# Kernel tuning notes

Hardware: AMD Instinct MI355X
Metric: run time of the kernel (lower is better)

Reference implementation:

```python
import jax, jax.numpy as jnp
import numpy as np
from jax import lax

C_IN = 256
C_OUT = 256
KS = 3


def _conv(x, w, b):
    # x: [B,C,H,W], w: [O,I,kh,kw] -> NCHW 'SAME' conv, stride 1
    y = lax.conv_general_dilated(x, w, window_strides=(1, 1), padding='SAME',
                                 dimension_numbers=('NCHW', 'OIHW', 'NCHW'))
    return y + b[None, :, None, None]


def setup_inputs() -> dict:
    key = jax.random.key(0)
    ks = jax.random.split(key, 7)
    B, H, W = 2, 64, 64
    fan = C_IN * KS * KS
    lim = float(np.sqrt(6.0 / (fan + C_OUT * KS * KS)))  # xavier uniform
    return {
        'x': jax.random.normal(ks[0], (B, C_IN, H, W), jnp.float32),
        'ref_x': jax.random.normal(ks[1], (B, C_IN, H, W), jnp.float32),
        'conv1_w': jax.random.uniform(ks[2], (C_OUT, C_IN, KS, KS), jnp.float32, -lim, lim),
        'conv1_b': jnp.zeros((C_OUT,), jnp.float32),
        'conv2_w': jax.random.uniform(ks[3], (C_OUT, C_IN, KS, KS), jnp.float32, -lim, lim),
        'conv2_b': jnp.zeros((C_OUT,), jnp.float32),
        'gamma': jnp.array([0.5], jnp.float32),
    }


def reference(x, ref_x, conv1_w, conv1_b, conv2_w, conv2_b, gamma):
    B, Cin, H, W = x.shape
    HW = H * W
    x_f = jax.nn.relu(_conv(x, conv1_w, conv1_b)).reshape(B, C_OUT, HW)        # [B,C,HW]
    r_f = jax.nn.relu(_conv(ref_x, conv1_w, conv1_b))                          # [B,C,H,W]
    r_f = r_f.transpose(0, 2, 3, 1).reshape(B, HW, C_OUT)                      # [B,HW,C]
    corr = jnp.einsum('bnc,bcm->bnm', r_f, x_f)                                # [B,HW,HW]
    corr = jax.nn.softmax(corr, axis=1)                                        # softmax over ref positions
    ref_c2 = jax.nn.relu(_conv(x, conv2_w, conv2_b)).reshape(B, C_OUT, HW)     # [B,C,HW]
    A = jnp.einsum('bcn,bnm->bcm', ref_c2, corr).reshape(x.shape)              # [B,C,H,W]
    return A * gamma[0] + x
```

## Files before the change

kernel.cpp:

```cpp
#include <hip/hip_runtime.h>
#include <hip/hip_bf16.h>

#define B_ 2
#define C_ 256
#define H_ 64
#define W_ 64
#define N_ 4096

typedef short bf16x8 __attribute__((ext_vector_type(8)));
typedef _Float16 f16x8 __attribute__((ext_vector_type(8)));
typedef float f32x4 __attribute__((ext_vector_type(4)));
typedef float f32x16 __attribute__((ext_vector_type(16)));

static __device__ __forceinline__ unsigned short f2bf(float f) {
    union { float f; unsigned u; } uf; uf.f = f;
    unsigned r = uf.u + 0x7fffu + ((uf.u >> 16) & 1u);
    return (unsigned short)(r >> 16);
}
static __device__ __forceinline__ unsigned short f2h_u(float f) {
    union { _Float16 h; unsigned short u; } c; c.h = (_Float16)f; return c.u;
}

static __device__ __forceinline__ void gload16(const void* g, void* l) {
    __builtin_amdgcn_global_load_lds(
        (const __attribute__((address_space(1))) unsigned int*)g,
        (__attribute__((address_space(3))) unsigned int*)l, 16, 0, 0);
}

__global__ __launch_bounds__(256) void cvt_x_k(const float* __restrict__ x,
                                               const float* __restrict__ ref_x,
                                               unsigned short* __restrict__ xtx,
                                               unsigned short* __restrict__ xtr)
{
    __shared__ unsigned short t[64][72];
    const int pt = blockIdx.x, ct = blockIdx.y;
    const int which = blockIdx.z >> 1, b = blockIdx.z & 1;
    const float* in = which ? ref_x : x;
    unsigned short* out = which ? xtr : xtx;
    const int a = threadIdx.x & 63, r = threadIdx.x >> 6;
    #pragma unroll
    for (int i = 0; i < 16; ++i) {
        int c = i * 4 + r;
        t[c][a] = f2h_u(in[((size_t)(b * C_ + ct * 64 + c) << 12) + pt * 64 + a]);
    }
    __syncthreads();
    #pragma unroll
    for (int i = 0; i < 16; ++i) {
        int p = i * 4 + r;
        out[((size_t)(b * N_ + pt * 64 + p) << 8) + ct * 64 + a] = t[a][p];
    }
}

__global__ __launch_bounds__(256) void cvt_w_k(const float* __restrict__ w1,
                                               const float* __restrict__ w2,
                                               unsigned short* __restrict__ wh1,
                                               unsigned short* __restrict__ wh2)
{
    int g = blockIdx.x;
    const float* w = (g < 2304) ? w1 : w2;
    unsigned short* wh = (g < 2304) ? wh1 : wh2;
    int i = (g % 2304) * 256 + threadIdx.x;
    int ci = i & 255, co = (i >> 8) & 255, tap = i >> 16;
    wh[i] = f2h_u(w[((size_t)(co * 256 + ci)) * 9 + tap]);
}

__global__ __launch_bounds__(256) void conv_mfma_k(
    const unsigned short* __restrict__ xtx, const unsigned short* __restrict__ xtr,
    const unsigned short* __restrict__ w1h, const unsigned short* __restrict__ w2h,
    const float* __restrict__ b1, const float* __restrict__ b2,
    unsigned short* __restrict__ f1x, unsigned short* __restrict__ f1r,
    unsigned short* __restrict__ f2)
{
    __shared__ unsigned short As[4 * 576 * 8];
    __shared__ unsigned short Bs[4 * 66 * 32];
    const int tid = threadIdx.x;
    const int pt  = blockIdx.x;
    const int cot = blockIdx.y;
    const int cid = blockIdx.z >> 1;
    const int b   = blockIdx.z & 1;

    const unsigned short* xt = (cid == 1) ? xtr : xtx;
    const unsigned short* wt = (cid == 2) ? w2h : w1h;
    const float* bias = (cid == 2) ? b2 : b1;
    unsigned short* out = (cid == 0) ? f1x : (cid == 1) ? f1r : f2;
    const int trans = (cid != 2);

    const int lane = tid & 63, wid = tid >> 6;
    const int wco = wid >> 1, wpos = wid & 1;
    const int rl = lane & 15, q = lane >> 4;
    const int r0 = pt * 2;

    f32x4 acc[2][4];
    #pragma unroll
    for (int mi = 0; mi < 2; ++mi)
        #pragma unroll
        for (int ni = 0; ni < 4; ++ni)
            #pragma unroll
            for (int e = 0; e < 4; ++e) acc[mi][ni][e] = 0.f;

    for (int k0 = 0; k0 < C_; k0 += 32) {
        #pragma unroll
        for (int tap = 0; tap < 9; ++tap) {
            gload16(wt + ((size_t)(tap * C_ + cot * 64 + lane) << 8) + k0 + wid * 8,
                    &As[(wid * 576 + tap * 64 + lane) * 8]);
        }
        #pragma unroll
        for (int j = 0; j < 5; ++j) {
            int it = tid + j * 256;
            if (it < 1056) {
                int col = it >> 4, sub = it & 15;
                int row = sub >> 2, qb = sub & 3;
                int h = r0 + row - 1, c = col - 1;
                float4 v; v.x = 0.f; v.y = 0.f; v.z = 0.f; v.w = 0.f;
                if (h >= 0 && h < 64 && c >= 0 && c < 64)
                    v = *(const float4*)(xt + ((size_t)(b * N_ + h * 64 + c) << 8) + k0 + qb * 8);
                int chunk = qb ^ ((col >> 1) & 3);
                *(float4*)&Bs[(row * 66 + col) * 32 + chunk * 8] = v;
            }
        }
        __syncthreads();

        #pragma unroll
        for (int tap = 0; tap < 9; ++tap) {
            const int kh = tap / 3, kw = tap % 3;
            f16x8 a0 = *(const f16x8*)&As[(q * 576 + tap * 64 + wco * 32 + rl) * 8];
            f16x8 a1 = *(const f16x8*)&As[(q * 576 + tap * 64 + wco * 32 + 16 + rl) * 8];
            const int chunkB = q ^ (((rl + kw) >> 1) & 3);
            const int rowB = (wpos + kh) * 66;
            #pragma unroll
            for (int ni = 0; ni < 4; ++ni) {
                int colB = ni * 16 + rl + kw;
                f16x8 bf = *(const f16x8*)&Bs[(rowB + colB) * 32 + chunkB * 8];
                acc[0][ni] = __builtin_amdgcn_mfma_f32_16x16x32_f16(a0, bf, acc[0][ni], 0, 0, 0);
                acc[1][ni] = __builtin_amdgcn_mfma_f32_16x16x32_f16(a1, bf, acc[1][ni], 0, 0, 0);
            }
        }
        __syncthreads();
    }

    #pragma unroll
    for (int mi = 0; mi < 2; ++mi) {
        const int co = cot * 64 + wco * 32 + mi * 16 + q * 4;
        float bs[4];
        #pragma unroll
        for (int rr = 0; rr < 4; ++rr) bs[rr] = bias[co + rr];
        #pragma unroll
        for (int ni = 0; ni < 4; ++ni) {
            const int pos = pt * 128 + wpos * 64 + ni * 16 + rl;
            if (trans) {
                unsigned short pk[4];
                #pragma unroll
                for (int rr = 0; rr < 4; ++rr)
                    pk[rr] = f2bf(fmaxf(acc[mi][ni][rr] + bs[rr], 0.f));
                uint2 u;
                u.x = (unsigned)pk[0] | ((unsigned)pk[1] << 16);
                u.y = (unsigned)pk[2] | ((unsigned)pk[3] << 16);
                *(uint2*)&out[((size_t)(b * N_ + pos) << 8) + co] = u;
            } else {
                #pragma unroll
                for (int rr = 0; rr < 4; ++rr)
                    out[((size_t)(b * C_ + co + rr) << 12) + pos] =
                        f2bf(fmaxf(acc[mi][ni][rr] + bs[rr], 0.f));
            }
        }
    }
}

__global__ __launch_bounds__(256, 2) void flash_k(
    const unsigned short* __restrict__ f1x,
    const unsigned short* __restrict__ f1r,
    const unsigned short* __restrict__ f2,
    float* __restrict__ part,
    float* __restrict__ stats)
{
    __shared__ unsigned short Ks[64 * 264];
    __shared__ unsigned short Vs[256 * 72];
    const int tid = threadIdx.x;
    const int mt = blockIdx.x, s = blockIdx.y, b = blockIdx.z;
    const int m0 = mt * 32;
    const int lane = tid & 63, wid = tid >> 6;
    const int wn = wid & 1, wc2 = wid >> 1;
    const int rl = lane & 31, l5 = lane >> 5;
    const int c0w = wc2 * 128;
    const int nw = wn * 32;

    bf16x8 Qf[16];
    #pragma unroll
    for (int st = 0; st < 16; ++st)
        Qf[st] = *(const bf16x8*)&f1x[(((size_t)b * N_ + m0 + rl) << 8) + st * 16 + l5 * 8];

    f32x16 O[4];
    #pragma unroll
    for (int cf = 0; cf < 4; ++cf)
        #pragma unroll
        for (int e = 0; e < 16; ++e) O[cf][e] = 0.f;
    float m_run = -1e30f, l_run = 0.f;

    const int nbase = s * 2048;
    for (int r = 0; r < 32; ++r) {
        const int n0 = nbase + r * 64;
        #pragma unroll
        for (int j = 0; j < 8; ++j) {
            int it = tid + j * 256;
            int n = it >> 5, cq = it & 31;
            *(float4*)&Ks[n * 264 + cq * 8] =
                *(const float4*)&f1r[(((size_t)b * N_ + n0 + n) << 8) + cq * 8];
        }
        #pragma unroll
        for (int j = 0; j < 8; ++j) {
            int it = tid + j * 256;
            int c = it >> 3, nq = it & 7;
            *(float4*)&Vs[c * 72 + nq * 8] =
                *(const float4*)&f2[(((size_t)b * C_ + c) << 12) + n0 + nq * 8];
        }
        __syncthreads();

        f32x16 S;
        #pragma unroll
        for (int e = 0; e < 16; ++e) S[e] = 0.f;
        __builtin_amdgcn_s_setprio(1);
        #pragma unroll
        for (int st = 0; st < 16; ++st) {
            bf16x8 Kf = *(const bf16x8*)&Ks[(nw + rl) * 264 + st * 16 + l5 * 8];
            S = __builtin_amdgcn_mfma_f32_32x32x16_bf16(Kf, Qf[st], S, 0, 0, 0);
        }
        __builtin_amdgcn_s_setprio(0);

        float mx = S[0];
        #pragma unroll
        for (int e = 1; e < 16; ++e) mx = fmaxf(mx, S[e]);
        mx = fmaxf(mx, __shfl_xor(mx, 32));
        float m_new = fmaxf(m_run, mx);
        float sc = __expf(m_run - m_new);
        float p[16]; float lsum = 0.f;
        #pragma unroll
        for (int e = 0; e < 16; ++e) { p[e] = __expf(S[e] - m_new); lsum += p[e]; }
        l_run = l_run * sc + lsum;
        m_run = m_new;
        #pragma unroll
        for (int cf = 0; cf < 4; ++cf)
            #pragma unroll
            for (int e = 0; e < 16; ++e) O[cf][e] *= sc;

        unsigned pk_[8], xk[8];
        #pragma unroll
        for (int g = 0; g < 8; ++g)
            pk_[g] = (unsigned)f2bf(p[2 * g]) | ((unsigned)f2bf(p[2 * g + 1]) << 16);
        #pragma unroll
        for (int g = 0; g < 8; ++g) xk[g] = (unsigned)__shfl_xor((int)pk_[g], 32);
        union { unsigned d[4]; bf16x8 v; } P0, P1;
        P0.d[0] = l5 ? xk[2] : pk_[0];
        P0.d[1] = l5 ? xk[3] : pk_[1];
        P0.d[2] = l5 ? pk_[2] : xk[0];
        P0.d[3] = l5 ? pk_[3] : xk[1];
        P1.d[0] = l5 ? xk[6] : pk_[4];
        P1.d[1] = l5 ? xk[7] : pk_[5];
        P1.d[2] = l5 ? pk_[6] : xk[4];
        P1.d[3] = l5 ? pk_[7] : xk[5];

        __builtin_amdgcn_s_setprio(1);
        #pragma unroll
        for (int cf = 0; cf < 4; ++cf) {
            const int vrow = (c0w + cf * 32 + rl) * 72;
            bf16x8 Vf0 = *(const bf16x8*)&Vs[vrow + nw + l5 * 8];
            O[cf] = __builtin_amdgcn_mfma_f32_32x32x16_bf16(Vf0, P0.v, O[cf], 0, 0, 0);
            bf16x8 Vf1 = *(const bf16x8*)&Vs[vrow + nw + 16 + l5 * 8];
            O[cf] = __builtin_amdgcn_mfma_f32_32x32x16_bf16(Vf1, P1.v, O[cf], 0, 0, 0);
        }
        __builtin_amdgcn_s_setprio(0);
        __syncthreads();
    }

    float l_tot = l_run + __shfl_xor(l_run, 32);
    const int se = s * 2 + wn;
    float* pb = part + (size_t)se * ((size_t)B_ * C_ * N_);
    #pragma unroll
    for (int cf = 0; cf < 4; ++cf)
        #pragma unroll
        for (int e = 0; e < 16; ++e) {
            int c = c0w + cf * 32 + (e & 3) + 8 * (e >> 2) + 4 * l5;
            pb[(((size_t)b * C_ + c) << 12) + m0 + rl] = O[cf][e];
        }
    if (wc2 == 0 && l5 == 0) {
        float2 st; st.x = m_run; st.y = l_tot;
        ((float2*)stats)[(((size_t)(se * 2 + b)) << 12) + m0 + rl] = st;
    }
}

__global__ __launch_bounds__(256) void combine_k(
    const float* __restrict__ part, const float* __restrict__ stats,
    const float* __restrict__ x, const float* __restrict__ gamma,
    float* __restrict__ out)
{
    const float g = gamma[0];
    size_t i = (size_t)blockIdx.x * 256 + threadIdx.x;
    size_t idx = i << 2;
    const int m = (int)(idx & 4095);
    const int b = (int)(idx >> 20);
    const size_t PS = (size_t)B_ * C_ * N_;

    float ms[4][4], ls[4][4];
    #pragma unroll
    for (int se = 0; se < 4; ++se) {
        const float2* sp = (const float2*)stats + (((size_t)(se * 2 + b)) << 12) + m;
        #pragma unroll
        for (int j = 0; j < 4; ++j) { float2 v = sp[j]; ms[se][j] = v.x; ls[se][j] = v.y; }
    }
    float w[4][4], den[4] = {0.f, 0.f, 0.f, 0.f};
    #pragma unroll
    for (int j = 0; j < 4; ++j) {
        float M = fmaxf(fmaxf(ms[0][j], ms[1][j]), fmaxf(ms[2][j], ms[3][j]));
        #pragma unroll
        for (int se = 0; se < 4; ++se) {
            w[se][j] = __expf(ms[se][j] - M);
            den[j] += w[se][j] * ls[se][j];
        }
    }
    float num[4] = {0.f, 0.f, 0.f, 0.f};
    #pragma unroll
    for (int se = 0; se < 4; ++se) {
        float4 p = *(const float4*)&part[se * PS + idx];
        num[0] += w[se][0] * p.x; num[1] += w[se][1] * p.y;
        num[2] += w[se][2] * p.z; num[3] += w[se][3] * p.w;
    }
    float4 xv = ((const float4*)x)[i];
    float4 o;
    o.x = g * num[0] / den[0] + xv.x;
    o.y = g * num[1] / den[1] + xv.y;
    o.z = g * num[2] / den[2] + xv.z;
    o.w = g * num[3] / den[3] + xv.w;
    ((float4*)out)[i] = o;
}

extern "C" void kernel_launch(void* const* d_in, const int* in_sizes, int n_in,
                              void* d_out, int out_size, void* d_ws, size_t ws_size,
                              hipStream_t stream) {
    const float* x     = (const float*)d_in[0];
    const float* ref_x = (const float*)d_in[1];
    const float* w1    = (const float*)d_in[2];
    const float* b1    = (const float*)d_in[3];
    const float* w2    = (const float*)d_in[4];
    const float* b2    = (const float*)d_in[5];
    const float* gamma = (const float*)d_in[6];
    float* out = (float*)d_out;

    char* ws = (char*)d_ws;
    size_t off = 0;
    auto nxt = [&](size_t bytes) {
        char* p = ws + off;
        off += (bytes + 255) & ~(size_t)255;
        return p;
    };
    unsigned short* f1x = (unsigned short*)nxt((size_t)B_ * N_ * C_ * 2);
    unsigned short* f1r = (unsigned short*)nxt((size_t)B_ * N_ * C_ * 2);
    unsigned short* f2  = (unsigned short*)nxt((size_t)B_ * N_ * C_ * 2);
    unsigned short* xtx = (unsigned short*)nxt((size_t)B_ * N_ * C_ * 2);
    unsigned short* xtr = (unsigned short*)nxt((size_t)B_ * N_ * C_ * 2);
    unsigned short* w1h = (unsigned short*)nxt((size_t)9 * C_ * C_ * 2);
    unsigned short* w2h = (unsigned short*)nxt((size_t)9 * C_ * C_ * 2);
    float* part  = (float*)nxt((size_t)4 * B_ * C_ * N_ * 4);
    float* stats = (float*)nxt((size_t)4 * B_ * N_ * 8);

    cvt_x_k<<<dim3(64, 4, 4), 256, 0, stream>>>(x, ref_x, xtx, xtr);
    cvt_w_k<<<4608, 256, 0, stream>>>(w1, w2, w1h, w2h);

    conv_mfma_k<<<dim3(32, 4, 6), 256, 0, stream>>>(xtx, xtr, w1h, w2h, b1, b2,
                                                    f1x, f1r, f2);

    flash_k<<<dim3(128, 2, 2), 256, 0, stream>>>(f1x, f1r, f2, part, stats);
    combine_k<<<2048, 256, 0, stream>>>(part, stats, x, gamma, out);
}
```

Baseline: 150.9 us.

## Widen flash query tile to 64, split keys 4 ways, alias partials into workspace

```diff
diff --git a/kernel.cpp b/kernel.cpp
--- a/kernel.cpp
+++ b/kernel.cpp
@@ -177,11 +177,10 @@
     __shared__ unsigned short Vs[256 * 72];
     const int tid = threadIdx.x;
     const int mt = blockIdx.x, s = blockIdx.y, b = blockIdx.z;
-    const int m0 = mt * 32;
     const int lane = tid & 63, wid = tid >> 6;
-    const int wn = wid & 1, wc2 = wid >> 1;
+    const int wm = wid >> 1, wn = wid & 1;
     const int rl = lane & 31, l5 = lane >> 5;
-    const int c0w = wc2 * 128;
+    const int m0 = mt * 64 + wm * 32;
     const int nw = wn * 32;
 
     bf16x8 Qf[16];
@@ -189,15 +188,15 @@
     for (int st = 0; st < 16; ++st)
         Qf[st] = *(const bf16x8*)&f1x[(((size_t)b * N_ + m0 + rl) << 8) + st * 16 + l5 * 8];
 
-    f32x16 O[4];
-    #pragma unroll
-    for (int cf = 0; cf < 4; ++cf)
+    f32x16 O[8];
+    #pragma unroll
+    for (int cf = 0; cf < 8; ++cf)
         #pragma unroll
         for (int e = 0; e < 16; ++e) O[cf][e] = 0.f;
     float m_run = -1e30f, l_run = 0.f;
 
-    const int nbase = s * 2048;
-    for (int r = 0; r < 32; ++r) {
+    const int nbase = s * 1024;
+    for (int r = 0; r < 16; ++r) {
         const int n0 = nbase + r * 64;
         #pragma unroll
         for (int j = 0; j < 8; ++j) {
@@ -238,7 +237,7 @@
         l_run = l_run * sc + lsum;
         m_run = m_new;
         #pragma unroll
-        for (int cf = 0; cf < 4; ++cf)
+        for (int cf = 0; cf < 8; ++cf)
             #pragma unroll
             for (int e = 0; e < 16; ++e) O[cf][e] *= sc;
 
@@ -260,8 +259,8 @@
 
         __builtin_amdgcn_s_setprio(1);
         #pragma unroll
-        for (int cf = 0; cf < 4; ++cf) {
-            const int vrow = (c0w + cf * 32 + rl) * 72;
+        for (int cf = 0; cf < 8; ++cf) {
+            const int vrow = (cf * 32 + rl) * 72;
             bf16x8 Vf0 = *(const bf16x8*)&Vs[vrow + nw + l5 * 8];
             O[cf] = __builtin_amdgcn_mfma_f32_32x32x16_bf16(Vf0, P0.v, O[cf], 0, 0, 0);
             bf16x8 Vf1 = *(const bf16x8*)&Vs[vrow + nw + 16 + l5 * 8];
@@ -275,13 +274,13 @@
     const int se = s * 2 + wn;
     float* pb = part + (size_t)se * ((size_t)B_ * C_ * N_);
     #pragma unroll
-    for (int cf = 0; cf < 4; ++cf)
+    for (int cf = 0; cf < 8; ++cf)
         #pragma unroll
         for (int e = 0; e < 16; ++e) {
-            int c = c0w + cf * 32 + (e & 3) + 8 * (e >> 2) + 4 * l5;
+            int c = cf * 32 + (e & 3) + 8 * (e >> 2) + 4 * l5;
             pb[(((size_t)b * C_ + c) << 12) + m0 + rl] = O[cf][e];
         }
-    if (wc2 == 0 && l5 == 0) {
+    if (l5 == 0) {
         float2 st; st.x = m_run; st.y = l_tot;
         ((float2*)stats)[(((size_t)(se * 2 + b)) << 12) + m0 + rl] = st;
     }
@@ -299,26 +298,28 @@
     const int b = (int)(idx >> 20);
     const size_t PS = (size_t)B_ * C_ * N_;
 
-    float ms[4][4], ls[4][4];
-    #pragma unroll
-    for (int se = 0; se < 4; ++se) {
-        const float2* sp = (const float2*)stats + (((size_t)(se * 2 + b)) << 12) + m;
-        #pragma unroll
-        for (int j = 0; j < 4; ++j) { float2 v = sp[j]; ms[se][j] = v.x; ls[se][j] = v.y; }
-    }
-    float w[4][4], den[4] = {0.f, 0.f, 0.f, 0.f};
+    float w[8][4], den[4];
     #pragma unroll
     for (int j = 0; j < 4; ++j) {
-        float M = fmaxf(fmaxf(ms[0][j], ms[1][j]), fmaxf(ms[2][j], ms[3][j]));
-        #pragma unroll
-        for (int se = 0; se < 4; ++se) {
-            w[se][j] = __expf(ms[se][j] - M);
-            den[j] += w[se][j] * ls[se][j];
+        float ms[8], ls[8];
+        #pragma unroll
+        for (int se = 0; se < 8; ++se) {
+            float2 v = ((const float2*)stats)[(((size_t)(se * 2 + b)) << 12) + m + j];
+            ms[se] = v.x; ls[se] = v.y;
+        }
+        float M = ms[0];
+        #pragma unroll
+        for (int se = 1; se < 8; ++se) M = fmaxf(M, ms[se]);
+        den[j] = 0.f;
+        #pragma unroll
+        for (int se = 0; se < 8; ++se) {
+            w[se][j] = __expf(ms[se] - M);
+            den[j] += w[se][j] * ls[se];
         }
     }
     float num[4] = {0.f, 0.f, 0.f, 0.f};
     #pragma unroll
-    for (int se = 0; se < 4; ++se) {
+    for (int se = 0; se < 8; ++se) {
         float4 p = *(const float4*)&part[se * PS + idx];
         num[0] += w[se][0] * p.x; num[1] += w[se][1] * p.y;
         num[2] += w[se][2] * p.z; num[3] += w[se][3] * p.w;
@@ -358,8 +359,9 @@
     unsigned short* xtr = (unsigned short*)nxt((size_t)B_ * N_ * C_ * 2);
     unsigned short* w1h = (unsigned short*)nxt((size_t)9 * C_ * C_ * 2);
     unsigned short* w2h = (unsigned short*)nxt((size_t)9 * C_ * C_ * 2);
-    float* part  = (float*)nxt((size_t)4 * B_ * C_ * N_ * 4);
-    float* stats = (float*)nxt((size_t)4 * B_ * N_ * 8);
+
+    float* part  = (float*)xtx;
+    float* stats = (float*)((char*)xtx + (size_t)8 * B_ * C_ * N_ * 4);
 
     cvt_x_k<<<dim3(64, 4, 4), 256, 0, stream>>>(x, ref_x, xtx, xtr);
     cvt_w_k<<<4608, 256, 0, stream>>>(w1, w2, w1h, w2h);
@@ -367,6 +369,6 @@
     conv_mfma_k<<<dim3(32, 4, 6), 256, 0, stream>>>(xtx, xtr, w1h, w2h, b1, b2,
                                                     f1x, f1r, f2);
 
-    flash_k<<<dim3(128, 2, 2), 256, 0, stream>>>(f1x, f1r, f2, part, stats);
+    flash_k<<<dim3(64, 4, 2), 256, 0, stream>>>(f1x, f1r, f2, part, stats);
     combine_k<<<2048, 256, 0, stream>>>(part, stats, x, gamma, out);
 }
```

Measured after the change: 200.7 us. +33.0%, slower.
